# Kernel optimization log

Hardware: AMD Instinct MI355X
Metric: run time of the kernel (lower is better)

Reference implementation:

```python
import jax, jax.numpy as jnp
import numpy as np
from jax import lax

# model dims (must match init_kwargs)
NB, E, G0, G1 = 1, 64, 32, 256          # num_blocks, embed_dim, grid rows, grid cols
DM, DIN, DS, DC, DTR = 2048, 4096, 16, 4, 128  # d_model, d_inner, d_state, d_conv, dt_rank
PS, ST, KD = (2, 16), (2, 16), (31, 31)
B, C, T = 8, 64, 4096


def setup_inputs() -> dict:
    key = jax.random.key(0)
    ks = jax.random.split(key, 4)
    rng = np.random.default_rng(0)

    def w(*s, fan=None):
        fan = fan if fan is not None else s[-1]
        return jnp.asarray((rng.standard_normal(s) / np.sqrt(fan)).astype(np.float32))

    # mamba_ssm-style dt bias init: softplus(bias) ~ Uniform-log in [1e-3, 0.1]
    dt = np.exp(rng.uniform(size=(NB, 2, DIN)) * (np.log(0.1) - np.log(1e-3)) + np.log(1e-3))
    dt = np.clip(dt, 1e-4, None)
    bdt = jnp.asarray((dt + np.log(-np.expm1(-dt))).astype(np.float32))
    A_log = jnp.asarray(np.broadcast_to(np.log(np.arange(1, DS + 1, dtype=np.float32)), (NB, 2, DIN, DS)).copy())

    return {
        'x': jax.random.normal(ks[0], (B, C, T), dtype=jnp.float32),
        'mask': jax.random.uniform(ks[1], (B, C, T)) < 0.5,
        'proj_w': w(E, 1, PS[0], PS[1], fan=PS[0] * PS[1]),
        'proj_b': jnp.zeros((E,), jnp.float32),
        'pos_embed': 0.02 * jax.random.normal(ks[2], (1, G1, DM), dtype=jnp.float32),
        'in_proj_w': w(NB, 2, 2 * DIN, DM, fan=DM),
        'conv_w': w(NB, 2, DIN, DC, fan=DC),
        'conv_b': jnp.zeros((NB, 2, DIN), jnp.float32),
        'x_proj_w': w(NB, 2, DTR + 2 * DS, DIN, fan=DIN),
        'dt_proj_w': w(NB, 2, DIN, DTR, fan=DTR),
        'dt_proj_b': bdt,
        'A_log': A_log,
        'Dp': jnp.ones((NB, 2, DIN), jnp.float32),
        'out_proj_w': w(NB, 2, DM, DIN, fan=DIN),
        'ln_g': jnp.ones((NB, DM), jnp.float32),
        'ln_b': jnp.zeros((NB, DM), jnp.float32),
        'dec_conv_w': w(1, 1, KD[0], KD[1], fan=KD[0] * KD[1]),
        'convT_w': w(E, 1, PS[0], PS[1], fan=E),
        'convT_b': jnp.zeros((1,), jnp.float32),
    }


def _layernorm(x, g, b, eps=1e-5):
    m = jnp.mean(x, -1, keepdims=True)
    v = jnp.var(x, -1, keepdims=True)
    return (x - m) * lax.rsqrt(v + eps) * g + b


def _mamba(h, Win, Wc, bc, Wx, Wdt, bdt, Alog, Dp, Wout):
    # h: [B, L, DM]; faithful port of mamba_ssm Mamba (selective scan reference path)
    xz = jnp.einsum('bld,ed->ble', h, Win)               # [B, L, 2*DIN]
    xc, z = jnp.split(xz, 2, axis=-1)
    xc = xc.swapaxes(1, 2)                               # [B, DIN, L]
    xc = lax.conv_general_dilated(xc, Wc[:, None, :], (1,), ((DC - 1, 0),),
                                  dimension_numbers=('NCH', 'OIH', 'NCH'),
                                  feature_group_count=DIN) + bc[None, :, None]
    u = jax.nn.silu(xc).swapaxes(1, 2)                   # [B, L, DIN]
    x_dbl = jnp.einsum('bld,ed->ble', u, Wx)             # [B, L, DTR+2*DS]
    dt = jax.nn.softplus(jnp.einsum('blr,dr->bld', x_dbl[..., :DTR], Wdt) + bdt)
    Bm = x_dbl[..., DTR:DTR + DS]                        # [B, L, DS]
    Cm = x_dbl[..., DTR + DS:]                           # [B, L, DS]
    A = -jnp.exp(Alog)                                   # [DIN, DS]

    def step(hst, inp):
        dt_t, B_t, C_t, u_t = inp                        # [B,DIN],[B,DS],[B,DS],[B,DIN]
        dA = jnp.exp(dt_t[..., None] * A)                # [B, DIN, DS]
        hst = hst * dA + (dt_t * u_t)[..., None] * B_t[:, None, :]
        return hst, jnp.einsum('bds,bs->bd', hst, C_t)

    h0 = jnp.zeros((h.shape[0], DIN, DS), h.dtype)
    xs = (dt.swapaxes(0, 1), Bm.swapaxes(0, 1), Cm.swapaxes(0, 1), u.swapaxes(0, 1))
    _, ys = lax.scan(step, h0, xs)
    y = ys.swapaxes(0, 1) + u * Dp                       # [B, L, DIN]
    y = y * jax.nn.silu(z)
    return jnp.einsum('bld,ed->ble', y, Wout)            # [B, L, DM]


def _forward(x, mask, proj_w, proj_b, pos_embed, in_proj_w, conv_w, conv_b,
             x_proj_w, dt_proj_w, dt_proj_b, A_log, Dp, out_proj_w,
             ln_g, ln_b, dec_conv_w, convT_w, convT_b):
    xm = jnp.where(mask, 0.0, x)                         # x_masked[mask] = 0
    p = lax.conv_general_dilated(xm[:, None], proj_w, ST, 'VALID',
                                 dimension_numbers=('NCHW', 'OIHW', 'NCHW'))
    p = p + proj_b[None, :, None, None]                  # [B, E, G0, G1]
    h = p.reshape(p.shape[0], E * G0, G1).transpose(0, 2, 1) + pos_embed  # [B, G1, DM]
    for i in range(NB):
        a_f = (in_proj_w[i, 0], conv_w[i, 0], conv_b[i, 0], x_proj_w[i, 0], dt_proj_w[i, 0],
               dt_proj_b[i, 0], A_log[i, 0], Dp[i, 0], out_proj_w[i, 0])
        a_r = (in_proj_w[i, 1], conv_w[i, 1], conv_b[i, 1], x_proj_w[i, 1], dt_proj_w[i, 1],
               dt_proj_b[i, 1], A_log[i, 1], Dp[i, 1], out_proj_w[i, 1])
        o = _mamba(h, *a_f) + jnp.flip(_mamba(jnp.flip(h, 1), *a_r), 1)  # bidirectional add
        h = _layernorm(h + o, ln_g[i], ln_b[i])
    # Decoder
    d = lax.conv_general_dilated(h[:, None], dec_conv_w, (1, 1),
                                 (((KD[0] - 1) // 2,) * 2, ((KD[1] - 1) // 2,) * 2),
                                 dimension_numbers=('NCHW', 'OIHW', 'NCHW'))
    d = d[:, 0].transpose(0, 2, 1).reshape(-1, E, G0, G1)
    # ConvTranspose2d(E->1, k=PS, stride=ST) as lhs-dilated conv with flipped kernel
    wct = jnp.flip(convT_w, (2, 3)).swapaxes(0, 1)       # [1, E, kh, kw]
    rec = lax.conv_general_dilated(d, wct, (1, 1),
                                   ((PS[0] - 1, PS[0] - 1), (PS[1] - 1, PS[1] - 1)),
                                   lhs_dilation=ST,
                                   dimension_numbers=('NCHW', 'OIHW', 'NCHW'))
    rec = rec + convT_b[None, :, None, None]
    return rec[:, 0], x                                  # (x_reconstructed, x_original)


def reference(x, mask, proj_w, proj_b, pos_embed, in_proj_w, conv_w, conv_b,
              x_proj_w, dt_proj_w, dt_proj_b, A_log, Dp, out_proj_w,
              ln_g, ln_b, dec_conv_w, convT_w, convT_b):
    return _forward(x, mask, proj_w, proj_b, pos_embed, in_proj_w, conv_w, conv_b,
                    x_proj_w, dt_proj_w, dt_proj_b, A_log, Dp, out_proj_w,
                    ln_g, ln_b, dec_conv_w, convT_w, convT_b)
```

## Files before the change

kernel.cpp:

```cpp
#include <hip/hip_runtime.h>
#include <hip/hip_bf16.h>
#include <math.h>

typedef unsigned short u16;
typedef __attribute__((ext_vector_type(8))) short bf16x8;
typedef __attribute__((ext_vector_type(4))) float f32x4;

__device__ __forceinline__ float b2f(u16 v) {
  unsigned u = ((unsigned)v) << 16;
  return __builtin_bit_cast(float, u);
}
__device__ __forceinline__ u16 f2b(float f) {
  unsigned u = __builtin_bit_cast(unsigned, f);
  unsigned r = u + 0x7fffu + ((u >> 16) & 1u);
  return (u16)(r >> 16);
}
__device__ __forceinline__ void gload_lds16(const u16* g, u16* l) {
  __builtin_amdgcn_global_load_lds(
      (const __attribute__((address_space(1))) void*)g,
      (__attribute__((address_space(3))) void*)l, 16, 0, 0);
}

__global__ __launch_bounds__(256) void cvt_bf16_k(const float* __restrict__ s,
                                                  u16* __restrict__ d, int n4) {
  int i = blockIdx.x * 256 + threadIdx.x;
  if (i < n4) {
    float4 v = ((const float4*)s)[i];
    ushort4 o;
    o.x = f2b(v.x); o.y = f2b(v.y); o.z = f2b(v.z); o.w = f2b(v.w);
    ((ushort4*)d)[i] = o;
  }
}

__global__ __launch_bounds__(256) void toeplitz_k(
    const float* __restrict__ kw, u16* __restrict__ tb)
{
  int i = blockIdx.x * 256 + threadIdx.x;
  if (i >= 31744) return;
  int k = i & 31, n = (i >> 5) & 15, h = (i >> 9) & 1, ki = i >> 10;
  int t = h * 32 + k - n;
  float v = (t >= 0 && t <= 30) ? kw[ki * 31 + t] : 0.f;
  tb[i] = f2b(v);
}

__global__ __launch_bounds__(256) void patchify_k(
    const float* __restrict__ x, const int* __restrict__ mask,
    const float* __restrict__ pw, const float* __restrict__ pb,
    const float* __restrict__ pos, float* __restrict__ h, u16* __restrict__ hb)
{
  int g1 = blockIdx.x, b = blockIdx.y, tid = threadIdx.x;
  __shared__ float sX[64 * 17];
  __shared__ float sW[2048];
  for (int i = tid; i < 64 * 16; i += 256) {
    int r = i >> 4, c = i & 15;
    int gi = (b * 64 + r) * 4096 + g1 * 16 + c;
    sX[r * 17 + c] = mask[gi] ? 0.f : x[gi];
  }
  for (int i = tid; i < 2048; i += 256) sW[i] = pw[i];
  __syncthreads();
  for (int m = tid; m < 2048; m += 256) {
    int e = m >> 5, g0 = m & 31;
    float acc = pb[e];
    const float* w = &sW[e * 32];
#pragma unroll
    for (int kh = 0; kh < 2; ++kh)
#pragma unroll
      for (int kw = 0; kw < 16; ++kw)
        acc += sX[(2 * g0 + kh) * 17 + kw] * w[kh * 16 + kw];
    float v = acc + pos[g1 * 2048 + m];
    long o = ((long)b * 256 + g1) * 2048 + m;
    h[o] = v;
    hb[o] = f2b(v);
  }
}

__global__ __launch_bounds__(512, 2) void gemm256_k(
    const u16* __restrict__ A0,
    const u16* __restrict__ B0, long bStride,
    u16* __restrict__ C0, long cStride,
    const float* __restrict__ cw,
    const float* __restrict__ cb,
    u16* __restrict__ ub)
{
  constexpr int K = 2048, N = 8192, LDA = 2048;
  __shared__ __align__(16) u16 lds[67584];
  u16* As = lds;
  u16* Bs = lds + 32768;
  const int dir = blockIdx.z;
  const u16* A = A0;
  const u16* B = B0 + (long)dir * bStride;
  u16* C = C0 + (long)dir * cStride;
  const int flip = dir;

  const int tid = threadIdx.x;
  const int wave = tid >> 6, lane = tid & 63;
  const int wr = wave >> 2, wc = wave & 3;
  const int bm = blockIdx.y * 256, bn = blockIdx.x * 256;
  const int lr = lane & 15, lq = lane >> 4;

  f32x4 acc[8][4];
#pragma unroll
  for (int i = 0; i < 8; ++i)
#pragma unroll
    for (int j = 0; j < 4; ++j) acc[i][j] = (f32x4){0.f, 0.f, 0.f, 0.f};

  auto stage = [&](int buf, int kt) {
    int k0 = kt << 6;
#pragma unroll
    for (int hf = 0; hf < 2; ++hf)
#pragma unroll
      for (int j = 0; j < 2; ++j) {
        int g = j * 512 + tid;
        int rl = hf * 128 + (g >> 3);
        int gr = (g & 7) ^ ((g >> 3) & 7);
        int ar = flip ? (bm + 255 - rl) : (bm + rl);
        gload_lds16(A + (long)ar * LDA + k0 + gr * 8,
                    &As[buf * 16384 + hf * 8192 + g * 8]);
        gload_lds16(B + (long)(bn + rl) * K + k0 + gr * 8,
                    &Bs[buf * 16384 + hf * 8192 + g * 8]);
      }
  };

  const int nk = K >> 6;
  stage(0, 0);
  for (int kt = 0; kt < nk; ++kt) {
    __builtin_amdgcn_s_barrier();
    __builtin_amdgcn_sched_barrier(0);
    if (kt + 1 < nk) {
      stage((kt + 1) & 1, kt + 1);
      asm volatile("s_waitcnt vmcnt(16)" ::: "memory");
    } else {
      asm volatile("s_waitcnt vmcnt(0)" ::: "memory");
    }
    __builtin_amdgcn_sched_barrier(0);
    __builtin_amdgcn_s_barrier();
    __builtin_amdgcn_sched_barrier(0);
    const int buf = kt & 1;
#pragma unroll
    for (int h = 0; h < 2; ++h) {
      bf16x8 av[8], bv[4];
#pragma unroll
      for (int i = 0; i < 8; ++i) {
        int row = wr * 128 + i * 16 + lr;
        av[i] = *(const bf16x8*)
            &As[buf * 16384 + ((row * 64 + h * 32 + lq * 8) ^ ((row & 7) << 3))];
      }
#pragma unroll
      for (int j = 0; j < 4; ++j) {
        int row = wc * 64 + j * 16 + lr;
        bv[j] = *(const bf16x8*)
            &Bs[buf * 16384 + ((row * 64 + h * 32 + lq * 8) ^ ((row & 7) << 3))];
      }
      __builtin_amdgcn_s_setprio(1);
#pragma unroll
      for (int i = 0; i < 8; ++i)
#pragma unroll
        for (int j = 0; j < 4; ++j)
          acc[i][j] = __builtin_amdgcn_mfma_f32_16x16x32_bf16(
              av[i], bv[j], acc[i][j], 0, 0, 0);
      __builtin_amdgcn_s_setprio(0);
    }
  }

  if (bn < 4096) {
    __syncthreads();
    u16* tile = lds;
#pragma unroll
    for (int i = 0; i < 8; ++i) {
      int r0 = wr * 128 + i * 16 + lq * 4;
#pragma unroll
      for (int j = 0; j < 4; ++j) {
        int col = wc * 64 + j * 16 + lr;
        f32x4 v = acc[i][j];
#pragma unroll
        for (int r = 0; r < 4; ++r)
          tile[(r0 + r) * 264 + col] = f2b(v[r]);
      }
    }
    __syncthreads();
    const int rgrp = tid >> 5, c8 = tid & 31;
    const int d0 = bn + c8 * 8;
    float wv0[8], wv1[8], wv2[8], wv3[8], cbv[8];
#pragma unroll
    for (int e = 0; e < 8; ++e) {
      const float4 wq = *(const float4*)(cw + ((long)dir * 4096 + d0 + e) * 4);
      wv0[e] = wq.x; wv1[e] = wq.y; wv2[e] = wq.z; wv3[e] = wq.w;
      cbv[e] = cb[dir * 4096 + d0 + e];
    }
    const int l0 = rgrp * 16;
    float w0[8], w1[8], w2[8];
#pragma unroll
    for (int e = 0; e < 8; ++e) { w0[e] = 0.f; w1[e] = 0.f; w2[e] = 0.f; }
    if (rgrp > 0) {
      bf16x8 t0 = *(const bf16x8*)&tile[(l0 - 3) * 264 + c8 * 8];
      bf16x8 t1 = *(const bf16x8*)&tile[(l0 - 2) * 264 + c8 * 8];
      bf16x8 t2 = *(const bf16x8*)&tile[(l0 - 1) * 264 + c8 * 8];
#pragma unroll
      for (int e = 0; e < 8; ++e) {
        w0[e] = b2f((u16)t0[e]); w1[e] = b2f((u16)t1[e]); w2[e] = b2f((u16)t2[e]);
      }
    }
    long ubase = ((long)(dir * 8 + blockIdx.y) * 256 + l0) * 4096 + d0;
#pragma unroll
    for (int l = 0; l < 16; ++l) {
      bf16x8 t = *(const bf16x8*)&tile[(l0 + l) * 264 + c8 * 8];
      float cur[8];
#pragma unroll
      for (int e = 0; e < 8; ++e) cur[e] = b2f((u16)t[e]);
      bf16x8 ov;
#pragma unroll
      for (int e = 0; e < 8; ++e) {
        float a = cbv[e] + wv0[e] * w0[e] + wv1[e] * w1[e] + wv2[e] * w2[e] +
                  wv3[e] * cur[e];
        ov[e] = (short)f2b(a / (1.f + __expf(-a)));
      }
      *(bf16x8*)(ub + ubase + (long)l * 4096) = ov;
#pragma unroll
      for (int e = 0; e < 8; ++e) { w0[e] = w1[e]; w1[e] = w2[e]; w2[e] = cur[e]; }
    }
  } else {
#pragma unroll
    for (int i = 0; i < 8; ++i) {
      int r0 = bm + wr * 128 + i * 16 + lq * 4;
#pragma unroll
      for (int j = 0; j < 4; ++j) {
        int col = bn + wc * 64 + j * 16 + lr;
        f32x4 v = acc[i][j];
#pragma unroll
        for (int r = 0; r < 4; ++r)
          C[(long)(r0 + r) * N + col] = f2b(v[r]);
      }
    }
  }
}

__global__ __launch_bounds__(512, 2) void gemm256o_k(
    const u16* __restrict__ Y0,
    const u16* __restrict__ W0,
    float* __restrict__ part)
{
  constexpr int LDK = 4096;
  __shared__ __align__(16) u16 lds[65536];
  u16* As = lds;
  u16* Bs = lds + 32768;
  const int dir = blockIdx.z >> 1, split = blockIdx.z & 1;
  const u16* A = Y0 + (long)dir * 2048 * 4096;
  const u16* B = W0 + (long)dir * 2048 * 4096;
  float* C = part + (long)blockIdx.z * 4194304;
  const int kbase = split << 11;

  const int tid = threadIdx.x;
  const int wave = tid >> 6, lane = tid & 63;
  const int wr = wave >> 2, wc = wave & 3;
  const int bm = blockIdx.y * 256, bn = blockIdx.x * 256;
  const int lr = lane & 15, lq = lane >> 4;

  f32x4 acc[8][4];
#pragma unroll
  for (int i = 0; i < 8; ++i)
#pragma unroll
    for (int j = 0; j < 4; ++j) acc[i][j] = (f32x4){0.f, 0.f, 0.f, 0.f};

  auto stage = [&](int buf, int kt) {
    int k0 = kbase + (kt << 6);
#pragma unroll
    for (int hf = 0; hf < 2; ++hf)
#pragma unroll
      for (int j = 0; j < 2; ++j) {
        int g = j * 512 + tid;
        int rl = hf * 128 + (g >> 3);
        int gr = (g & 7) ^ ((g >> 3) & 7);
        gload_lds16(A + (long)(bm + rl) * LDK + k0 + gr * 8,
                    &As[buf * 16384 + hf * 8192 + g * 8]);
        gload_lds16(B + (long)(bn + rl) * LDK + k0 + gr * 8,
                    &Bs[buf * 16384 + hf * 8192 + g * 8]);
      }
  };

  const int nk = 32;
  stage(0, 0);
  for (int kt = 0; kt < nk; ++kt) {
    __builtin_amdgcn_s_barrier();
    __builtin_amdgcn_sched_barrier(0);
    if (kt + 1 < nk) {
      stage((kt + 1) & 1, kt + 1);
      asm volatile("s_waitcnt vmcnt(16)" ::: "memory");
    } else {
      asm volatile("s_waitcnt vmcnt(0)" ::: "memory");
    }
    __builtin_amdgcn_sched_barrier(0);
    __builtin_amdgcn_s_barrier();
    __builtin_amdgcn_sched_barrier(0);
    const int buf = kt & 1;
#pragma unroll
    for (int h = 0; h < 2; ++h) {
      bf16x8 av[8], bv[4];
#pragma unroll
      for (int i = 0; i < 8; ++i) {
        int row = wr * 128 + i * 16 + lr;
        av[i] = *(const bf16x8*)
            &As[buf * 16384 + ((row * 64 + h * 32 + lq * 8) ^ ((row & 7) << 3))];
      }
#pragma unroll
      for (int j = 0; j < 4; ++j) {
        int row = wc * 64 + j * 16 + lr;
        bv[j] = *(const bf16x8*)
            &Bs[buf * 16384 + ((row * 64 + h * 32 + lq * 8) ^ ((row & 7) << 3))];
      }
      __builtin_amdgcn_s_setprio(1);
#pragma unroll
      for (int i = 0; i < 8; ++i)
#pragma unroll
        for (int j = 0; j < 4; ++j)
          acc[i][j] = __builtin_amdgcn_mfma_f32_16x16x32_bf16(
              av[i], bv[j], acc[i][j], 0, 0, 0);
      __builtin_amdgcn_s_setprio(0);
    }
  }

#pragma unroll
  for (int i = 0; i < 8; ++i) {
    int r0 = bm + wr * 128 + i * 16 + lq * 4;
#pragma unroll
    for (int j = 0; j < 4; ++j) {
      int col = bn + wc * 64 + j * 16 + lr;
      f32x4 v = acc[i][j];
#pragma unroll
      for (int r = 0; r < 4; ++r)
        C[(long)(r0 + r) * 2048 + col] = v[r];
    }
  }
}

__global__ __launch_bounds__(256) void oproj_reduce_k(
    const float* __restrict__ part, float* __restrict__ ob)
{
  int i = blockIdx.x * 256 + threadIdx.x;
  if (i >= 2097152) return;
  int dir = i >> 20, rem = i & 1048575;
  const float4* p0 = (const float4*)(part + (long)(dir * 2) * 4194304) + rem;
  const float4* p1 = (const float4*)(part + (long)(dir * 2 + 1) * 4194304) + rem;
  float4 a = *p0, b = *p1;
  ((float4*)(ob + (long)dir * 4194304))[rem] =
      make_float4(a.x + b.x, a.y + b.y, a.z + b.z, a.w + b.w);
}

template <int EPI, int F32OUT, int BFOUT>
__global__ __launch_bounds__(256) void mfma_gemm_k(
    const u16* __restrict__ A0, long aStride,
    const u16* __restrict__ B0, long bStride,
    float* __restrict__ C0, long cStride,
    u16* __restrict__ Cb0, long cbStride,
    const float* __restrict__ bias0, int biasStride,
    int N, int K, int lda, int flipDir1)
{
  __shared__ __align__(16) u16 As[2][4096];
  __shared__ __align__(16) u16 Bs[2][4096];
  const int dir = blockIdx.z;
  const u16* A = A0 + (long)dir * aStride;
  const u16* B = B0 + (long)dir * bStride;
  float* C = F32OUT ? (C0 + (long)dir * cStride) : nullptr;
  u16* Cb = BFOUT ? (Cb0 + (long)dir * cbStride) : nullptr;
  const float* bias = (EPI == 1) ? (bias0 + (long)dir * biasStride) : nullptr;
  const int flip = flipDir1 && (dir == 1);

  const int tid = threadIdx.x;
  const int wave = tid >> 6, lane = tid & 63;
  const int wr = wave >> 1, wc = wave & 1;
  const int bm = blockIdx.y * 128, bn = blockIdx.x * 128;
  const int lr = lane & 15, lq = lane >> 4;

  f32x4 acc[4][4];
#pragma unroll
  for (int i = 0; i < 4; ++i)
#pragma unroll
    for (int j = 0; j < 4; ++j) acc[i][j] = (f32x4){0.f, 0.f, 0.f, 0.f};

  const int nk = K >> 5;

  auto stage = [&](int buf, int k0) {
#pragma unroll
    for (int iss = 0; iss < 2; ++iss) {
      int ob = wave * 2048 + iss * 1024 + lane * 16;
      int row = ob >> 6, kb = (ob >> 4) & 3;
      int rg = bm + row;
      rg = flip ? ((rg & ~255) | (255 - (rg & 255))) : rg;
      gload_lds16(A + (long)rg * lda + k0 + kb * 8,
                  &As[buf][wave * 1024 + iss * 512]);
      int rb = bn + row; rb = (rb < N) ? rb : (N - 1);
      gload_lds16(B + (long)rb * K + k0 + kb * 8,
                  &Bs[buf][wave * 1024 + iss * 512]);
    }
  };

  stage(0, 0);
  for (int kt = 0; kt < nk; ++kt) {
    __syncthreads();
    if (kt + 1 < nk) stage((kt + 1) & 1, (kt + 1) << 5);
    const int buf = kt & 1;
    bf16x8 av[4], bv[4];
#pragma unroll
    for (int i = 0; i < 4; ++i)
      av[i] = *(const bf16x8*)&As[buf][(wr * 64 + i * 16 + lr) * 32 + lq * 8];
#pragma unroll
    for (int j = 0; j < 4; ++j)
      bv[j] = *(const bf16x8*)&Bs[buf][(wc * 64 + j * 16 + lr) * 32 + lq * 8];
#pragma unroll
    for (int i = 0; i < 4; ++i)
#pragma unroll
      for (int j = 0; j < 4; ++j)
        acc[i][j] = __builtin_amdgcn_mfma_f32_16x16x32_bf16(av[i], bv[j],
                                                            acc[i][j], 0, 0, 0);
  }

#pragma unroll
  for (int i = 0; i < 4; ++i) {
    int r0 = bm + wr * 64 + i * 16 + lq * 4;
#pragma unroll
    for (int j = 0; j < 4; ++j) {
      int col = bn + wc * 64 + j * 16 + lr;
      if (col < N) {
        f32x4 v = acc[i][j];
#pragma unroll
        for (int r = 0; r < 4; ++r) {
          float xv = v[r];
          if (EPI == 1) {
            xv += bias[col];
            xv = (xv > 20.f) ? xv : log1pf(expf(xv));
          }
          if (F32OUT) C[(long)(r0 + r) * N + col] = xv;
          if (BFOUT) Cb[(long)(r0 + r) * N + col] = f2b(xv);
        }
      }
    }
  }
}

__global__ __launch_bounds__(256) void xdbl_part_k(
    const u16* __restrict__ ubf, const u16* __restrict__ Wxbf,
    float* __restrict__ part)
{
  __shared__ __align__(16) u16 As[2][4096];
  __shared__ __align__(16) u16 Bs[2][4096];
  const int dir = blockIdx.z >> 2, split = blockIdx.z & 3;
  const u16* A = ubf + (long)dir * 2048 * 4096;
  const u16* B = Wxbf + (long)dir * 160 * 4096;
  float* C = part + (long)blockIdx.z * 327680;
  const int tid = threadIdx.x;
  const int wave = tid >> 6, lane = tid & 63;
  const int wr = wave >> 1, wc = wave & 1;
  const int bm = blockIdx.y * 128, bn = blockIdx.x * 128;
  const int lr = lane & 15, lq = lane >> 4;

  f32x4 acc[4][4];
#pragma unroll
  for (int i = 0; i < 4; ++i)
#pragma unroll
    for (int j = 0; j < 4; ++j) acc[i][j] = (f32x4){0.f, 0.f, 0.f, 0.f};

  auto stage = [&](int buf, int k0) {
#pragma unroll
    for (int iss = 0; iss < 2; ++iss) {
      int ob = wave * 2048 + iss * 1024 + lane * 16;
      int row = ob >> 6, kb = (ob >> 4) & 3;
      gload_lds16(A + (long)(bm + row) * 4096 + k0 + kb * 8,
                  &As[buf][wave * 1024 + iss * 512]);
      int rb = bn + row; rb = (rb < 160) ? rb : 159;
      gload_lds16(B + (long)rb * 4096 + k0 + kb * 8,
                  &Bs[buf][wave * 1024 + iss * 512]);
    }
  };

  const int kbase = split << 10;
  stage(0, kbase);
  for (int kt = 0; kt < 32; ++kt) {
    __syncthreads();
    if (kt + 1 < 32) stage((kt + 1) & 1, kbase + ((kt + 1) << 5));
    const int buf = kt & 1;
    bf16x8 av[4], bv[4];
#pragma unroll
    for (int i = 0; i < 4; ++i)
      av[i] = *(const bf16x8*)&As[buf][(wr * 64 + i * 16 + lr) * 32 + lq * 8];
#pragma unroll
    for (int j = 0; j < 4; ++j)
      bv[j] = *(const bf16x8*)&Bs[buf][(wc * 64 + j * 16 + lr) * 32 + lq * 8];
#pragma unroll
    for (int i = 0; i < 4; ++i)
#pragma unroll
      for (int j = 0; j < 4; ++j)
        acc[i][j] = __builtin_amdgcn_mfma_f32_16x16x32_bf16(av[i], bv[j],
                                                            acc[i][j], 0, 0, 0);
  }

#pragma unroll
  for (int i = 0; i < 4; ++i) {
    int r0 = bm + wr * 64 + i * 16 + lq * 4;
#pragma unroll
    for (int j = 0; j < 4; ++j) {
      int col = bn + wc * 64 + j * 16 + lr;
      if (col < 160) {
        f32x4 v = acc[i][j];
#pragma unroll
        for (int r = 0; r < 4; ++r)
          C[(long)(r0 + r) * 160 + col] = v[r];
      }
    }
  }
}

__global__ __launch_bounds__(256) void xdbl_reduce_k(
    const float* __restrict__ part, float* __restrict__ xdbl,
    u16* __restrict__ xdbl_bf)
{
  int i = blockIdx.x * 256 + threadIdx.x;
  if (i >= 655360) return;
  int dir = i / 327680, rem = i - dir * 327680;
  long pb = (long)dir * 4 * 327680 + rem;
  float s = part[pb] + part[pb + 327680] + part[pb + 2 * 327680] +
            part[pb + 3 * 327680];
  xdbl[i] = s;
  xdbl_bf[i] = f2b(s);
}

__global__ __launch_bounds__(256) void scan_a_k(
    const u16* __restrict__ dtbuf, const u16* __restrict__ ubuf,
    const float* __restrict__ xdbl, const float* __restrict__ A_log,
    const float* __restrict__ Dpv, u16* __restrict__ ypre,
    float* __restrict__ stend, float* __restrict__ dtsum)
{
  int blk = blockIdx.x;
  int dtile = blk & 15, c = (blk >> 4) & 7, b = (blk >> 7) & 7, dir = blk >> 10;
  int tid = threadIdx.x;
  int d = dtile * 256 + tid;
  int db = dir * 8 + b;

  __shared__ float sB[32][16], sC[32][16];
  long r160 = (long)db * 256 * 160;
  for (int i = tid; i < 1024; i += 256) {
    int l = i >> 5, s = i & 31;
    float v = xdbl[r160 + (long)(c * 32 + l) * 160 + 128 + s];
    if (s < 16) sB[l][s] = v; else sC[l][s - 16] = v;
  }
  __syncthreads();

  float A[16], st[16];
  const float4* ap = (const float4*)(A_log + ((long)dir * 4096 + d) * 16);
#pragma unroll
  for (int q = 0; q < 4; ++q) {
    float4 t = ap[q];
    A[q * 4 + 0] = -__expf(t.x); A[q * 4 + 1] = -__expf(t.y);
    A[q * 4 + 2] = -__expf(t.z); A[q * 4 + 3] = -__expf(t.w);
  }
#pragma unroll
  for (int s = 0; s < 16; ++s) st[s] = 0.f;
  float Dpd = Dpv[dir * 4096 + d];

  long base = (long)db * 256 * 4096 + (long)c * 32 * 4096 + d;
  float dts = 0.f;
  for (int i = 0; i < 32; ++i) {
    float dtv = b2f(dtbuf[base + (long)i * 4096]);
    float uv  = b2f(ubuf[base + (long)i * 4096]);
    dts += dtv;
    float du = dtv * uv;
    float y = 0.f;
#pragma unroll
    for (int s = 0; s < 16; ++s) {
      st[s] = st[s] * __expf(dtv * A[s]) + du * sB[i][s];
      y += st[s] * sC[i][s];
    }
    ypre[base + (long)i * 4096] = f2b(y + uv * Dpd);
  }
  long eb = ((long)(db * 8 + c) * 4096 + d) * 16;
  float4* ep = (float4*)(stend + eb);
#pragma unroll
  for (int q = 0; q < 4; ++q)
    ep[q] = make_float4(st[q * 4], st[q * 4 + 1], st[q * 4 + 2], st[q * 4 + 3]);
  dtsum[(long)(db * 8 + c) * 4096 + d] = dts;
}

__global__ __launch_bounds__(512) void scan_b_k(
    const u16* __restrict__ dtbuf, const u16* __restrict__ xzbf,
    const float* __restrict__ xdbl, const float* __restrict__ A_log,
    const float* __restrict__ stend, const float* __restrict__ dtsum,
    u16* __restrict__ ybuf)
{
  int blk = blockIdx.x;
  int dtile = blk & 63, b = (blk >> 6) & 7, dir = blk >> 9;
  int tid = threadIdx.x;
  int c = tid >> 6, dd = tid & 63;
  int d0 = dtile * 64, d = d0 + dd;
  int db = dir * 8 + b;

  __shared__ float sEnd[8][64][17];
  __shared__ float sT[8][64];
  __shared__ float sC[256][16];

  long eBase = (long)db * 8 * 65536;
  for (int i = tid; i < 8192; i += 512) {
    int cc = i >> 10, rem = i & 1023, dd2 = rem >> 4, s = rem & 15;
    sEnd[cc][dd2][s] = stend[eBase + (long)cc * 65536 + (long)(d0 + dd2) * 16 + s];
  }
  {
    int cc = tid >> 6, dd2 = tid & 63;
    sT[cc][dd2] = dtsum[(long)(db * 8 + cc) * 4096 + d0 + dd2];
  }
  long r160 = (long)db * 256 * 160;
  for (int i = tid; i < 4096; i += 512) {
    int l = i >> 4, s = i & 15;
    sC[l][s] = xdbl[r160 + (long)l * 160 + 144 + s];
  }
  __syncthreads();

  float A[16];
  const float4* ap = (const float4*)(A_log + ((long)dir * 4096 + d) * 16);
#pragma unroll
  for (int q = 0; q < 4; ++q) {
    float4 t = ap[q];
    A[q * 4 + 0] = -__expf(t.x); A[q * 4 + 1] = -__expf(t.y);
    A[q * 4 + 2] = -__expf(t.z); A[q * 4 + 3] = -__expf(t.w);
  }
  float g[16];
#pragma unroll
  for (int s = 0; s < 16; ++s) g[s] = 0.f;
  for (int j = 0; j < c; ++j) {
    float Tj = sT[j][dd];
#pragma unroll
    for (int s = 0; s < 16; ++s)
      g[s] = g[s] * __expf(A[s] * Tj) + sEnd[j][dd][s];
  }

  long base  = (long)db * 256 * 4096 + (long)c * 32 * 4096 + d;
  long zbase = (long)db * 256 * 8192 + (long)c * 32 * 8192 + 4096 + d;
  float cum = 0.f;
  if (c == 0) {
    for (int i = 0; i < 32; ++i) {
      float yp = b2f(ybuf[base + (long)i * 4096]);
      float zv = b2f(xzbf[zbase + (long)i * 8192]);
      float y = yp * (zv / (1.f + __expf(-zv)));
      ybuf[base + (long)i * 4096] = f2b(y);
    }
  } else {
    for (int i = 0; i < 32; ++i) {
      float dtv = b2f(dtbuf[base + (long)i * 4096]);
      cum += dtv;
      float yp = b2f(ybuf[base + (long)i * 4096]);
      float corr = 0.f;
      const int l = c * 32 + i;
#pragma unroll
      for (int s = 0; s < 16; ++s)
        corr += sC[l][s] * __expf(A[s] * cum) * g[s];
      float zv = b2f(xzbf[zbase + (long)i * 8192]);
      float y = (yp + corr) * (zv / (1.f + __expf(-zv)));
      ybuf[base + (long)i * 4096] = f2b(y);
    }
  }
}

__global__ __launch_bounds__(256) void add_ln_k(
    const float* __restrict__ h, const float* __restrict__ o0,
    const float* __restrict__ o1, const float* __restrict__ g,
    const float* __restrict__ bta, float* __restrict__ h2)
{
  int row = blockIdx.x;
  int b = row >> 8, l = row & 255;
  long base = (long)row * 2048;
  long base1 = ((long)b * 256 + (255 - l)) * 2048;
  int t8 = threadIdx.x * 8;
  float v[8];
  float4 x0 = *(const float4*)(h + base + t8);
  float4 x1 = *(const float4*)(h + base + t8 + 4);
  float4 a0 = *(const float4*)(o0 + base + t8);
  float4 a1 = *(const float4*)(o0 + base + t8 + 4);
  float4 c0 = *(const float4*)(o1 + base1 + t8);
  float4 c1 = *(const float4*)(o1 + base1 + t8 + 4);
  v[0] = x0.x + a0.x + c0.x; v[1] = x0.y + a0.y + c0.y;
  v[2] = x0.z + a0.z + c0.z; v[3] = x0.w + a0.w + c0.w;
  v[4] = x1.x + a1.x + c1.x; v[5] = x1.y + a1.y + c1.y;
  v[6] = x1.z + a1.z + c1.z; v[7] = x1.w + a1.w + c1.w;
  float s = 0.f, ss = 0.f;
#pragma unroll
  for (int j = 0; j < 8; ++j) { s += v[j]; ss += v[j] * v[j]; }
#pragma unroll
  for (int off = 32; off >= 1; off >>= 1) {
    s += __shfl_xor(s, off, 64);
    ss += __shfl_xor(ss, off, 64);
  }
  __shared__ float red[8];
  int wid = threadIdx.x >> 6, lane = threadIdx.x & 63;
  if (lane == 0) { red[wid] = s; red[wid + 4] = ss; }
  __syncthreads();
  if (threadIdx.x == 0) {
    red[0] = red[0] + red[1] + red[2] + red[3];
    red[4] = red[4] + red[5] + red[6] + red[7];
  }
  __syncthreads();
  float mean = red[0] * (1.f / 2048.f);
  float var = red[4] * (1.f / 2048.f) - mean * mean;
  float inv = rsqrtf(var + 1e-5f);
  float o[8];
#pragma unroll
  for (int j = 0; j < 8; ++j)
    o[j] = (v[j] - mean) * inv * g[t8 + j] + bta[t8 + j];
  *(float4*)(h2 + base + t8) = make_float4(o[0], o[1], o[2], o[3]);
  *(float4*)(h2 + base + t8 + 4) = make_float4(o[4], o[5], o[6], o[7]);
}

__global__ __launch_bounds__(256) void dec_conv31_k(
    const float* __restrict__ h2, const u16* __restrict__ tb,
    float* __restrict__ dc)
{
  __shared__ __align__(16) u16 sIn[94 * 120];
  const int b = blockIdx.z;
  const int l0 = blockIdx.y * 64;
  const int m0 = blockIdx.x * 64;
  const int tid = threadIdx.x;
  const float* src = h2 + (long)b * 256 * 2048;
  for (int i = tid; i < 94 * 112; i += 256) {
    int r = i / 112, c = i - r * 112;
    int gl = l0 + r - 15, gm = m0 + c - 15;
    float v = 0.f;
    if (gl >= 0 && gl < 256 && gm >= 0 && gm < 2048)
      v = src[(long)gl * 2048 + gm];
    sIn[r * 120 + c] = f2b(v);
  }
  __syncthreads();
  const int wave = tid >> 6, lane = tid & 63;
  const int lr = lane & 15, lq = lane >> 4;

  f32x4 acc[4];
#pragma unroll
  for (int s = 0; s < 4; ++s) acc[s] = (f32x4){0.f, 0.f, 0.f, 0.f};

#pragma unroll 1
  for (int ki = 0; ki < 31; ++ki) {
    const u16* arow = &sIn[(wave * 16 + lr + ki) * 120];
#pragma unroll
    for (int h = 0; h < 2; ++h) {
      bf16x8 bv = *(const bf16x8*)&tb[((ki * 2 + h) * 16 + lr) * 32 + lq * 8];
#pragma unroll
      for (int ms = 0; ms < 4; ++ms) {
        bf16x8 av = *(const bf16x8*)&arow[ms * 16 + h * 32 + lq * 8];
        acc[ms] = __builtin_amdgcn_mfma_f32_16x16x32_bf16(av, bv, acc[ms], 0, 0, 0);
      }
    }
  }
#pragma unroll
  for (int ms = 0; ms < 4; ++ms) {
    f32x4 v = acc[ms];
#pragma unroll
    for (int r = 0; r < 4; ++r)
      dc[((long)b * 256 + l0 + wave * 16 + lq * 4 + r) * 2048 + m0 + ms * 16 + lr]
          = v[r];
  }
}

__global__ __launch_bounds__(256) void convT_k(
    const float* __restrict__ dc, const float* __restrict__ w,
    const float* __restrict__ wb, float* __restrict__ out)
{
  int j = blockIdx.x, b = blockIdx.y;
  __shared__ float sD[2048];
  __shared__ float sW[2048];
  int tid = threadIdx.x;
  const float* drow = dc + ((long)b * 256 + j) * 2048;
  for (int i = tid; i < 2048; i += 256) { sD[i] = drow[i]; sW[i] = w[i]; }
  __syncthreads();
  float cb = wb[0];
  int owlo = tid & 15, ohbase = tid >> 4;
#pragma unroll
  for (int q = 0; q < 4; ++q) {
    int oh = ohbase + q * 16;
    int i = oh >> 1, a = oh & 1;
    float acc = cb;
#pragma unroll 8
    for (int e = 0; e < 64; ++e)
      acc += sD[e * 32 + i] * sW[e * 32 + a * 16 + owlo];
    out[((long)b * 64 + oh) * 4096 + j * 16 + owlo] = acc;
  }
}

extern "C" void kernel_launch(void* const* d_in, const int* in_sizes, int n_in,
                              void* d_out, int out_size, void* d_ws, size_t ws_size,
                              hipStream_t stream)
{
  const float* x      = (const float*)d_in[0];
  const int*   mask   = (const int*)d_in[1];
  const float* proj_w = (const float*)d_in[2];
  const float* proj_b = (const float*)d_in[3];
  const float* pos    = (const float*)d_in[4];
  const float* Wip    = (const float*)d_in[5];
  const float* convw  = (const float*)d_in[6];
  const float* convb  = (const float*)d_in[7];
  const float* Wx     = (const float*)d_in[8];
  const float* Wdt    = (const float*)d_in[9];
  const float* bdt    = (const float*)d_in[10];
  const float* Alog   = (const float*)d_in[11];
  const float* Dpv    = (const float*)d_in[12];
  const float* Wout   = (const float*)d_in[13];
  const float* lng    = (const float*)d_in[14];
  const float* lnb    = (const float*)d_in[15];
  const float* dkw    = (const float*)d_in[16];
  const float* ctw    = (const float*)d_in[17];
  const float* ctb    = (const float*)d_in[18];
  float* out = (float*)d_out;

  char* p = (char*)d_ws;
  u16*   xz_bf   = (u16*)p;
  float* ob      = (float*)p;
  p += 67108864;
  u16*   u_bf    = (u16*)p;
  float* dc      = (float*)p;
  p += 33554432;
  u16*   dt_bf   = (u16*)p; p += 67108864;
  float* xdbl    = (float*)p; p += 2621440;
  u16*   xdbl_bf = (u16*)p;  p += 1310720;
  float* h       = (float*)p; p += 16777216;
  u16*   h_bf    = (u16*)p;  p += 8388608;
  float* h2      = (float*)p; p += 16777216;
  u16*   y_bf    = (u16*)p;  p += 33554432;
  u16*   Wpool   = (u16*)p;  p += 67108864;
  u16*   Wx_bf   = (u16*)p;  p += 2621440;
  u16*   Wdt_bf  = (u16*)p;  p += 2097152;
  u16*   tb      = (u16*)p;  p += 65536;

  float* part    = (float*)(Wpool + 16777216);
  float* st_end  = (float*)(Wpool + 16777216);
  float* dtsum   = h2;
  float* opart   = (float*)dt_bf;

  cvt_bf16_k<<<32768, 256, 0, stream>>>(Wip, Wpool, 8388608);
  cvt_bf16_k<<<1280, 256, 0, stream>>>(Wx, Wx_bf, 327680);
  cvt_bf16_k<<<1024, 256, 0, stream>>>(Wdt, Wdt_bf, 262144);
  toeplitz_k<<<124, 256, 0, stream>>>(dkw, tb);

  patchify_k<<<dim3(256, 8), 256, 0, stream>>>(x, mask, proj_w, proj_b, pos, h, h_bf);

  gemm256_k<<<dim3(32, 8, 2), 512, 0, stream>>>(
      h_bf, Wpool, (long)8192 * 2048, xz_bf, (long)2048 * 8192,
      convw, convb, u_bf);

  xdbl_part_k<<<dim3(2, 16, 8), 256, 0, stream>>>(u_bf, Wx_bf, part);
  xdbl_reduce_k<<<2560, 256, 0, stream>>>(part, xdbl, xdbl_bf);

  mfma_gemm_k<1, 0, 1><<<dim3(32, 16, 2), 256, 0, stream>>>(
      xdbl_bf, (long)2048 * 160, Wdt_bf, (long)4096 * 128, nullptr, 0L,
      dt_bf, (long)2048 * 4096, bdt, 4096, 4096, 128, 160, 0);

  scan_a_k<<<2048, 256, 0, stream>>>(dt_bf, u_bf, xdbl, Alog, Dpv, y_bf, st_end, dtsum);
  scan_b_k<<<1024, 512, 0, stream>>>(dt_bf, xz_bf, xdbl, Alog, st_end, dtsum, y_bf);

  cvt_bf16_k<<<16384, 256, 0, stream>>>(Wout, Wpool, 4194304);

  gemm256o_k<<<dim3(8, 8, 4), 512, 0, stream>>>(y_bf, Wpool, opart);
  oproj_reduce_k<<<8192, 256, 0, stream>>>(opart, ob);

  add_ln_k<<<2048, 256, 0, stream>>>(h, ob, ob + (long)2048 * 2048, lng, lnb, h2);

  dec_conv31_k<<<dim3(32, 4, 8), 256, 0, stream>>>(h2, tb, dc);

  convT_k<<<dim3(256, 8), 256, 0, stream>>>(dc, ctw, ctb, out);

  hipMemcpyAsync(out + 2097152, x, (size_t)2097152 * 4,
                 hipMemcpyDeviceToDevice, stream);
}
```

Before: 623.9 us.

## Halve in-proj GEMM LDS tile, fuse o-proj split-K reduce into layernorm, bf16 LN output

The in-proj GEMM now stages K-tiles of 32 instead of 64 with a new swizzle, which halves its shared memory so more blocks can be resident per CU. Its conv/SiLU epilogue is split into two halves, with a small side buffer carrying the three boundary rows between them. The separate o-proj partial-sum reduce kernel is removed, and the layernorm now reads all four partial buffers directly. The layernorm also writes bf16, which the decoder conv loads without converting. The trade-off is twice as many K-loop iterations and barriers in the GEMM, plus an extra synchronization phase in the epilogue.

```diff
diff --git a/kernel.cpp b/kernel.cpp
--- a/kernel.cpp
+++ b/kernel.cpp
@@ -83,9 +83,9 @@
     u16* __restrict__ ub)
 {
   constexpr int K = 2048, N = 8192, LDA = 2048;
-  __shared__ __align__(16) u16 lds[67584];
+  __shared__ __align__(16) u16 lds[34584];
   u16* As = lds;
-  u16* Bs = lds + 32768;
+  u16* Bs = lds + 16384;
   const int dir = blockIdx.z;
   const u16* A = A0;
   const u16* B = B0 + (long)dir * bStride;
@@ -105,30 +105,27 @@
     for (int j = 0; j < 4; ++j) acc[i][j] = (f32x4){0.f, 0.f, 0.f, 0.f};
 
   auto stage = [&](int buf, int kt) {
-    int k0 = kt << 6;
-#pragma unroll
-    for (int hf = 0; hf < 2; ++hf)
-#pragma unroll
-      for (int j = 0; j < 2; ++j) {
-        int g = j * 512 + tid;
-        int rl = hf * 128 + (g >> 3);
-        int gr = (g & 7) ^ ((g >> 3) & 7);
-        int ar = flip ? (bm + 255 - rl) : (bm + rl);
-        gload_lds16(A + (long)ar * LDA + k0 + gr * 8,
-                    &As[buf * 16384 + hf * 8192 + g * 8]);
-        gload_lds16(B + (long)(bn + rl) * K + k0 + gr * 8,
-                    &Bs[buf * 16384 + hf * 8192 + g * 8]);
-      }
+    int k0 = kt << 5;
+#pragma unroll
+    for (int j = 0; j < 2; ++j) {
+      int g = j * 512 + tid;
+      int row = g >> 2, sp = g & 3;
+      int ss = sp ^ (row & 3) ^ (((row >> 2) & 1) << 1);
+      int ar = flip ? (bm + 255 - row) : (bm + row);
+      gload_lds16(A + (long)ar * LDA + k0 + ss * 8, &As[buf * 8192 + g * 8]);
+      gload_lds16(B + (long)(bn + row) * K + k0 + ss * 8,
+                  &Bs[buf * 8192 + g * 8]);
+    }
   };
 
-  const int nk = K >> 6;
+  const int nk = K >> 5;
   stage(0, 0);
   for (int kt = 0; kt < nk; ++kt) {
     __builtin_amdgcn_s_barrier();
     __builtin_amdgcn_sched_barrier(0);
     if (kt + 1 < nk) {
       stage((kt + 1) & 1, kt + 1);
-      asm volatile("s_waitcnt vmcnt(16)" ::: "memory");
+      asm volatile("s_waitcnt vmcnt(4)" ::: "memory");
     } else {
       asm volatile("s_waitcnt vmcnt(0)" ::: "memory");
     }
@@ -136,48 +133,32 @@
     __builtin_amdgcn_s_barrier();
     __builtin_amdgcn_sched_barrier(0);
     const int buf = kt & 1;
-#pragma unroll
-    for (int h = 0; h < 2; ++h) {
-      bf16x8 av[8], bv[4];
-#pragma unroll
-      for (int i = 0; i < 8; ++i) {
-        int row = wr * 128 + i * 16 + lr;
-        av[i] = *(const bf16x8*)
-            &As[buf * 16384 + ((row * 64 + h * 32 + lq * 8) ^ ((row & 7) << 3))];
-      }
-#pragma unroll
-      for (int j = 0; j < 4; ++j) {
-        int row = wc * 64 + j * 16 + lr;
-        bv[j] = *(const bf16x8*)
-            &Bs[buf * 16384 + ((row * 64 + h * 32 + lq * 8) ^ ((row & 7) << 3))];
-      }
-      __builtin_amdgcn_s_setprio(1);
-#pragma unroll
-      for (int i = 0; i < 8; ++i)
-#pragma unroll
-        for (int j = 0; j < 4; ++j)
-          acc[i][j] = __builtin_amdgcn_mfma_f32_16x16x32_bf16(
-              av[i], bv[j], acc[i][j], 0, 0, 0);
-      __builtin_amdgcn_s_setprio(0);
-    }
+    bf16x8 av[8], bv[4];
+#pragma unroll
+    for (int i = 0; i < 8; ++i) {
+      int R = wr * 128 + i * 16 + lr;
+      int gp = lq ^ (R & 3) ^ (((R >> 2) & 1) << 1);
+      av[i] = *(const bf16x8*)&As[buf * 8192 + R * 32 + gp * 8];
+    }
+#pragma unroll
+    for (int j = 0; j < 4; ++j) {
+      int R = wc * 64 + j * 16 + lr;
+      int gp = lq ^ (R & 3) ^ (((R >> 2) & 1) << 1);
+      bv[j] = *(const bf16x8*)&Bs[buf * 8192 + R * 32 + gp * 8];
+    }
+    __builtin_amdgcn_s_setprio(1);
+#pragma unroll
+    for (int i = 0; i < 8; ++i)
+#pragma unroll
+      for (int j = 0; j < 4; ++j)
+        acc[i][j] = __builtin_amdgcn_mfma_f32_16x16x32_bf16(
+            av[i], bv[j], acc[i][j], 0, 0, 0);
+    __builtin_amdgcn_s_setprio(0);
   }
 
   if (bn < 4096) {
-    __syncthreads();
     u16* tile = lds;
-#pragma unroll
-    for (int i = 0; i < 8; ++i) {
-      int r0 = wr * 128 + i * 16 + lq * 4;
-#pragma unroll
-      for (int j = 0; j < 4; ++j) {
-        int col = wc * 64 + j * 16 + lr;
-        f32x4 v = acc[i][j];
-#pragma unroll
-        for (int r = 0; r < 4; ++r)
-          tile[(r0 + r) * 264 + col] = f2b(v[r]);
-      }
-    }
-    __syncthreads();
+    u16* side = lds + 33792;
     const int rgrp = tid >> 5, c8 = tid & 31;
     const int d0 = bn + c8 * 8;
     float wv0[8], wv1[8], wv2[8], wv3[8], cbv[8];
@@ -187,37 +168,83 @@
       wv0[e] = wq.x; wv1[e] = wq.y; wv2[e] = wq.z; wv3[e] = wq.w;
       cbv[e] = cb[dir * 4096 + d0 + e];
     }
-    const int l0 = rgrp * 16;
     float w0[8], w1[8], w2[8];
-#pragma unroll
-    for (int e = 0; e < 8; ++e) { w0[e] = 0.f; w1[e] = 0.f; w2[e] = 0.f; }
-    if (rgrp > 0) {
-      bf16x8 t0 = *(const bf16x8*)&tile[(l0 - 3) * 264 + c8 * 8];
-      bf16x8 t1 = *(const bf16x8*)&tile[(l0 - 2) * 264 + c8 * 8];
-      bf16x8 t2 = *(const bf16x8*)&tile[(l0 - 1) * 264 + c8 * 8];
-#pragma unroll
-      for (int e = 0; e < 8; ++e) {
-        w0[e] = b2f((u16)t0[e]); w1[e] = b2f((u16)t1[e]); w2[e] = b2f((u16)t2[e]);
-      }
-    }
-    long ubase = ((long)(dir * 8 + blockIdx.y) * 256 + l0) * 4096 + d0;
-#pragma unroll
-    for (int l = 0; l < 16; ++l) {
-      bf16x8 t = *(const bf16x8*)&tile[(l0 + l) * 264 + c8 * 8];
-      float cur[8];
-#pragma unroll
-      for (int e = 0; e < 8; ++e) cur[e] = b2f((u16)t[e]);
-      bf16x8 ov;
-#pragma unroll
-      for (int e = 0; e < 8; ++e) {
-        float a = cbv[e] + wv0[e] * w0[e] + wv1[e] * w1[e] + wv2[e] * w2[e] +
-                  wv3[e] * cur[e];
-        ov[e] = (short)f2b(a / (1.f + __expf(-a)));
-      }
-      *(bf16x8*)(ub + ubase + (long)l * 4096) = ov;
-#pragma unroll
-      for (int e = 0; e < 8; ++e) { w0[e] = w1[e]; w1[e] = w2[e]; w2[e] = cur[e]; }
-    }
+
+    auto writeacc = [&]() {
+#pragma unroll
+      for (int i = 0; i < 8; ++i) {
+        int r0 = i * 16 + lq * 4;
+#pragma unroll
+        for (int j = 0; j < 4; ++j) {
+          int col = wc * 64 + j * 16 + lr;
+          f32x4 v = acc[i][j];
+#pragma unroll
+          for (int r = 0; r < 4; ++r)
+            tile[(r0 + r) * 264 + col] = f2b(v[r]);
+        }
+      }
+    };
+
+    auto convhalf = [&](int hh) {
+      if (rgrp == 0) {
+        if (hh == 0) {
+#pragma unroll
+          for (int e = 0; e < 8; ++e) { w0[e] = 0.f; w1[e] = 0.f; w2[e] = 0.f; }
+        } else {
+          bf16x8 t0 = *(const bf16x8*)&side[0 * 264 + c8 * 8];
+          bf16x8 t1 = *(const bf16x8*)&side[1 * 264 + c8 * 8];
+          bf16x8 t2 = *(const bf16x8*)&side[2 * 264 + c8 * 8];
+#pragma unroll
+          for (int e = 0; e < 8; ++e) {
+            w0[e] = b2f((u16)t0[e]); w1[e] = b2f((u16)t1[e]);
+            w2[e] = b2f((u16)t2[e]);
+          }
+        }
+      } else {
+        int lb = rgrp * 8;
+        bf16x8 t0 = *(const bf16x8*)&tile[(lb - 3) * 264 + c8 * 8];
+        bf16x8 t1 = *(const bf16x8*)&tile[(lb - 2) * 264 + c8 * 8];
+        bf16x8 t2 = *(const bf16x8*)&tile[(lb - 1) * 264 + c8 * 8];
+#pragma unroll
+        for (int e = 0; e < 8; ++e) {
+          w0[e] = b2f((u16)t0[e]); w1[e] = b2f((u16)t1[e]);
+          w2[e] = b2f((u16)t2[e]);
+        }
+      }
+      long ubase = ((long)(dir * 8 + blockIdx.y) * 256 + hh * 128 + rgrp * 8)
+                       * 4096 + d0;
+#pragma unroll
+      for (int l = 0; l < 8; ++l) {
+        bf16x8 t = *(const bf16x8*)&tile[(rgrp * 8 + l) * 264 + c8 * 8];
+        float cur[8];
+#pragma unroll
+        for (int e = 0; e < 8; ++e) cur[e] = b2f((u16)t[e]);
+        bf16x8 ov;
+#pragma unroll
+        for (int e = 0; e < 8; ++e) {
+          float a = cbv[e] + wv0[e] * w0[e] + wv1[e] * w1[e] + wv2[e] * w2[e] +
+                    wv3[e] * cur[e];
+          ov[e] = (short)f2b(a / (1.f + __expf(-a)));
+        }
+        *(bf16x8*)(ub + ubase + (long)l * 4096) = ov;
+#pragma unroll
+        for (int e = 0; e < 8; ++e) { w0[e] = w1[e]; w1[e] = w2[e]; w2[e] = cur[e]; }
+      }
+    };
+
+    __syncthreads();
+    if (wr == 0) writeacc();
+    __syncthreads();
+    convhalf(0);
+    if (tid < 96) {
+      int rr = tid >> 5, cc = tid & 31;
+      *(bf16x8*)&side[rr * 264 + cc * 8] =
+          *(const bf16x8*)&tile[(125 + rr) * 264 + cc * 8];
+    }
+    __syncthreads();
+    if (wr == 1) writeacc();
+    __syncthreads();
+    convhalf(1);
   } else {
 #pragma unroll
     for (int i = 0; i < 8; ++i) {
@@ -330,19 +357,6 @@
         C[(long)(r0 + r) * 2048 + col] = v[r];
     }
   }
-}
-
-__global__ __launch_bounds__(256) void oproj_reduce_k(
-    const float* __restrict__ part, float* __restrict__ ob)
-{
-  int i = blockIdx.x * 256 + threadIdx.x;
-  if (i >= 2097152) return;
-  int dir = i >> 20, rem = i & 1048575;
-  const float4* p0 = (const float4*)(part + (long)(dir * 2) * 4194304) + rem;
-  const float4* p1 = (const float4*)(part + (long)(dir * 2 + 1) * 4194304) + rem;
-  float4 a = *p0, b = *p1;
-  ((float4*)(ob + (long)dir * 4194304))[rem] =
-      make_float4(a.x + b.x, a.y + b.y, a.z + b.z, a.w + b.w);
 }
 
 template <int EPI, int F32OUT, int BFOUT>
@@ -657,26 +671,38 @@
 }
 
 __global__ __launch_bounds__(256) void add_ln_k(
-    const float* __restrict__ h, const float* __restrict__ o0,
-    const float* __restrict__ o1, const float* __restrict__ g,
-    const float* __restrict__ bta, float* __restrict__ h2)
+    const float* __restrict__ h, const float* __restrict__ op,
+    const float* __restrict__ g, const float* __restrict__ bta,
+    u16* __restrict__ h2b)
 {
   int row = blockIdx.x;
   int b = row >> 8, l = row & 255;
   long base = (long)row * 2048;
   long base1 = ((long)b * 256 + (255 - l)) * 2048;
   int t8 = threadIdx.x * 8;
+  const float* p0 = op;
+  const float* p1 = op + 4194304;
+  const float* p2 = op + 2L * 4194304;
+  const float* p3 = op + 3L * 4194304;
   float v[8];
   float4 x0 = *(const float4*)(h + base + t8);
   float4 x1 = *(const float4*)(h + base + t8 + 4);
-  float4 a0 = *(const float4*)(o0 + base + t8);
-  float4 a1 = *(const float4*)(o0 + base + t8 + 4);
-  float4 c0 = *(const float4*)(o1 + base1 + t8);
-  float4 c1 = *(const float4*)(o1 + base1 + t8 + 4);
-  v[0] = x0.x + a0.x + c0.x; v[1] = x0.y + a0.y + c0.y;
-  v[2] = x0.z + a0.z + c0.z; v[3] = x0.w + a0.w + c0.w;
-  v[4] = x1.x + a1.x + c1.x; v[5] = x1.y + a1.y + c1.y;
-  v[6] = x1.z + a1.z + c1.z; v[7] = x1.w + a1.w + c1.w;
+  float4 a0 = *(const float4*)(p0 + base + t8);
+  float4 a1 = *(const float4*)(p0 + base + t8 + 4);
+  float4 b0 = *(const float4*)(p1 + base + t8);
+  float4 b1 = *(const float4*)(p1 + base + t8 + 4);
+  float4 c0 = *(const float4*)(p2 + base1 + t8);
+  float4 c1 = *(const float4*)(p2 + base1 + t8 + 4);
+  float4 d0 = *(const float4*)(p3 + base1 + t8);
+  float4 d1 = *(const float4*)(p3 + base1 + t8 + 4);
+  v[0] = x0.x + a0.x + b0.x + c0.x + d0.x;
+  v[1] = x0.y + a0.y + b0.y + c0.y + d0.y;
+  v[2] = x0.z + a0.z + b0.z + c0.z + d0.z;
+  v[3] = x0.w + a0.w + b0.w + c0.w + d0.w;
+  v[4] = x1.x + a1.x + b1.x + c1.x + d1.x;
+  v[5] = x1.y + a1.y + b1.y + c1.y + d1.y;
+  v[6] = x1.z + a1.z + b1.z + c1.z + d1.z;
+  v[7] = x1.w + a1.w + b1.w + c1.w + d1.w;
   float s = 0.f, ss = 0.f;
 #pragma unroll
   for (int j = 0; j < 8; ++j) { s += v[j]; ss += v[j] * v[j]; }
@@ -697,16 +723,15 @@
   float mean = red[0] * (1.f / 2048.f);
   float var = red[4] * (1.f / 2048.f) - mean * mean;
   float inv = rsqrtf(var + 1e-5f);
-  float o[8];
+  bf16x8 o;
 #pragma unroll
   for (int j = 0; j < 8; ++j)
-    o[j] = (v[j] - mean) * inv * g[t8 + j] + bta[t8 + j];
-  *(float4*)(h2 + base + t8) = make_float4(o[0], o[1], o[2], o[3]);
-  *(float4*)(h2 + base + t8 + 4) = make_float4(o[4], o[5], o[6], o[7]);
+    o[j] = (short)f2b((v[j] - mean) * inv * g[t8 + j] + bta[t8 + j]);
+  *(bf16x8*)(h2b + base + t8) = o;
 }
 
 __global__ __launch_bounds__(256) void dec_conv31_k(
-    const float* __restrict__ h2, const u16* __restrict__ tb,
+    const u16* __restrict__ h2b, const u16* __restrict__ tb,
     float* __restrict__ dc)
 {
   __shared__ __align__(16) u16 sIn[94 * 120];
@@ -714,14 +739,14 @@
   const int l0 = blockIdx.y * 64;
   const int m0 = blockIdx.x * 64;
   const int tid = threadIdx.x;
-  const float* src = h2 + (long)b * 256 * 2048;
+  const u16* src = h2b + (long)b * 256 * 2048;
   for (int i = tid; i < 94 * 112; i += 256) {
     int r = i / 112, c = i - r * 112;
     int gl = l0 + r - 15, gm = m0 + c - 15;
-    float v = 0.f;
+    u16 v = 0;
     if (gl >= 0 && gl < 256 && gm >= 0 && gm < 2048)
       v = src[(long)gl * 2048 + gm];
-    sIn[r * 120 + c] = f2b(v);
+    sIn[r * 120 + c] = v;
   }
   __syncthreads();
   const int wave = tid >> 6, lane = tid & 63;
@@ -806,7 +831,6 @@
 
   char* p = (char*)d_ws;
   u16*   xz_bf   = (u16*)p;
-  float* ob      = (float*)p;
   p += 67108864;
   u16*   u_bf    = (u16*)p;
   float* dc      = (float*)p;
@@ -822,6 +846,7 @@
   u16*   Wx_bf   = (u16*)p;  p += 2621440;
   u16*   Wdt_bf  = (u16*)p;  p += 2097152;
   u16*   tb      = (u16*)p;  p += 65536;
+  u16*   h2b     = (u16*)p;  p += 8388608;
 
   float* part    = (float*)(Wpool + 16777216);
   float* st_end  = (float*)(Wpool + 16777216);
@@ -852,11 +877,10 @@
   cvt_bf16_k<<<16384, 256, 0, stream>>>(Wout, Wpool, 4194304);
 
   gemm256o_k<<<dim3(8, 8, 4), 512, 0, stream>>>(y_bf, Wpool, opart);
-  oproj_reduce_k<<<8192, 256, 0, stream>>>(opart, ob);
-
-  add_ln_k<<<2048, 256, 0, stream>>>(h, ob, ob + (long)2048 * 2048, lng, lnb, h2);
-
-  dec_conv31_k<<<dim3(32, 4, 8), 256, 0, stream>>>(h2, tb, dc);
+
+  add_ln_k<<<2048, 256, 0, stream>>>(h, opart, lng, lnb, h2b);
+
+  dec_conv31_k<<<dim3(32, 4, 8), 256, 0, stream>>>(h2b, tb, dc);
 
   convT_k<<<dim3(256, 8), 256, 0, stream>>>(dc, ctw, ctb, out);
 
```

Result: no change. 616.6 us (-1.2%).

## Write out-proj partials as bf16 and fold split-K reduce into add+LayerNorm

Applied to the files above, without the earlier changes.

The split-K out-projection GEMM now stores its four partial outputs in bf16 instead of fp32. The separate reduce kernel is removed, and add_ln_k sums the residual plus all four partials directly. LayerNorm output is written as bf16, so the decoder conv loads bf16 without converting. This cuts one launch and several tens of MB of fp32 memory traffic, at the cost of extra rounding on the partial sums and on the LayerNorm output.

```diff
diff --git a/kernel.cpp b/kernel.cpp
--- a/kernel.cpp
+++ b/kernel.cpp
@@ -237,7 +237,7 @@
 __global__ __launch_bounds__(512, 2) void gemm256o_k(
     const u16* __restrict__ Y0,
     const u16* __restrict__ W0,
-    float* __restrict__ part)
+    u16* __restrict__ part)
 {
   constexpr int LDK = 4096;
   __shared__ __align__(16) u16 lds[65536];
@@ -246,7 +246,7 @@
   const int dir = blockIdx.z >> 1, split = blockIdx.z & 1;
   const u16* A = Y0 + (long)dir * 2048 * 4096;
   const u16* B = W0 + (long)dir * 2048 * 4096;
-  float* C = part + (long)blockIdx.z * 4194304;
+  u16* C = part + (long)blockIdx.z * 4194304;
   const int kbase = split << 11;
 
   const int tid = threadIdx.x;
@@ -327,22 +327,9 @@
       f32x4 v = acc[i][j];
 #pragma unroll
       for (int r = 0; r < 4; ++r)
-        C[(long)(r0 + r) * 2048 + col] = v[r];
-    }
-  }
-}
-
-__global__ __launch_bounds__(256) void oproj_reduce_k(
-    const float* __restrict__ part, float* __restrict__ ob)
-{
-  int i = blockIdx.x * 256 + threadIdx.x;
-  if (i >= 2097152) return;
-  int dir = i >> 20, rem = i & 1048575;
-  const float4* p0 = (const float4*)(part + (long)(dir * 2) * 4194304) + rem;
-  const float4* p1 = (const float4*)(part + (long)(dir * 2 + 1) * 4194304) + rem;
-  float4 a = *p0, b = *p1;
-  ((float4*)(ob + (long)dir * 4194304))[rem] =
-      make_float4(a.x + b.x, a.y + b.y, a.z + b.z, a.w + b.w);
+        C[(long)(r0 + r) * 2048 + col] = f2b(v[r]);
+    }
+  }
 }
 
 template <int EPI, int F32OUT, int BFOUT>
@@ -657,26 +644,33 @@
 }
 
 __global__ __launch_bounds__(256) void add_ln_k(
-    const float* __restrict__ h, const float* __restrict__ o0,
-    const float* __restrict__ o1, const float* __restrict__ g,
-    const float* __restrict__ bta, float* __restrict__ h2)
+    const float* __restrict__ h, const u16* __restrict__ op,
+    const float* __restrict__ g, const float* __restrict__ bta,
+    u16* __restrict__ h2b)
 {
   int row = blockIdx.x;
   int b = row >> 8, l = row & 255;
   long base = (long)row * 2048;
   long base1 = ((long)b * 256 + (255 - l)) * 2048;
   int t8 = threadIdx.x * 8;
+  const u16* p0 = op;
+  const u16* p1 = op + 4194304;
+  const u16* p2 = op + 2L * 4194304;
+  const u16* p3 = op + 3L * 4194304;
   float v[8];
   float4 x0 = *(const float4*)(h + base + t8);
   float4 x1 = *(const float4*)(h + base + t8 + 4);
-  float4 a0 = *(const float4*)(o0 + base + t8);
-  float4 a1 = *(const float4*)(o0 + base + t8 + 4);
-  float4 c0 = *(const float4*)(o1 + base1 + t8);
-  float4 c1 = *(const float4*)(o1 + base1 + t8 + 4);
-  v[0] = x0.x + a0.x + c0.x; v[1] = x0.y + a0.y + c0.y;
-  v[2] = x0.z + a0.z + c0.z; v[3] = x0.w + a0.w + c0.w;
-  v[4] = x1.x + a1.x + c1.x; v[5] = x1.y + a1.y + c1.y;
-  v[6] = x1.z + a1.z + c1.z; v[7] = x1.w + a1.w + c1.w;
+  bf16x8 a8 = *(const bf16x8*)(p0 + base + t8);
+  bf16x8 b8 = *(const bf16x8*)(p1 + base + t8);
+  bf16x8 c8v = *(const bf16x8*)(p2 + base1 + t8);
+  bf16x8 d8 = *(const bf16x8*)(p3 + base1 + t8);
+  const float* xp = (const float*)&x0;
+  float xv[8] = {x0.x, x0.y, x0.z, x0.w, x1.x, x1.y, x1.z, x1.w};
+  (void)xp;
+#pragma unroll
+  for (int j = 0; j < 8; ++j)
+    v[j] = xv[j] + b2f((u16)a8[j]) + b2f((u16)b8[j]) + b2f((u16)c8v[j]) +
+           b2f((u16)d8[j]);
   float s = 0.f, ss = 0.f;
 #pragma unroll
   for (int j = 0; j < 8; ++j) { s += v[j]; ss += v[j] * v[j]; }
@@ -697,16 +691,15 @@
   float mean = red[0] * (1.f / 2048.f);
   float var = red[4] * (1.f / 2048.f) - mean * mean;
   float inv = rsqrtf(var + 1e-5f);
-  float o[8];
+  bf16x8 o;
 #pragma unroll
   for (int j = 0; j < 8; ++j)
-    o[j] = (v[j] - mean) * inv * g[t8 + j] + bta[t8 + j];
-  *(float4*)(h2 + base + t8) = make_float4(o[0], o[1], o[2], o[3]);
-  *(float4*)(h2 + base + t8 + 4) = make_float4(o[4], o[5], o[6], o[7]);
+    o[j] = (short)f2b((v[j] - mean) * inv * g[t8 + j] + bta[t8 + j]);
+  *(bf16x8*)(h2b + base + t8) = o;
 }
 
 __global__ __launch_bounds__(256) void dec_conv31_k(
-    const float* __restrict__ h2, const u16* __restrict__ tb,
+    const u16* __restrict__ h2b, const u16* __restrict__ tb,
     float* __restrict__ dc)
 {
   __shared__ __align__(16) u16 sIn[94 * 120];
@@ -714,14 +707,14 @@
   const int l0 = blockIdx.y * 64;
   const int m0 = blockIdx.x * 64;
   const int tid = threadIdx.x;
-  const float* src = h2 + (long)b * 256 * 2048;
+  const u16* src = h2b + (long)b * 256 * 2048;
   for (int i = tid; i < 94 * 112; i += 256) {
     int r = i / 112, c = i - r * 112;
     int gl = l0 + r - 15, gm = m0 + c - 15;
-    float v = 0.f;
+    u16 v = 0;
     if (gl >= 0 && gl < 256 && gm >= 0 && gm < 2048)
       v = src[(long)gl * 2048 + gm];
-    sIn[r * 120 + c] = f2b(v);
+    sIn[r * 120 + c] = v;
   }
   __syncthreads();
   const int wave = tid >> 6, lane = tid & 63;
@@ -806,7 +799,6 @@
 
   char* p = (char*)d_ws;
   u16*   xz_bf   = (u16*)p;
-  float* ob      = (float*)p;
   p += 67108864;
   u16*   u_bf    = (u16*)p;
   float* dc      = (float*)p;
@@ -822,11 +814,12 @@
   u16*   Wx_bf   = (u16*)p;  p += 2621440;
   u16*   Wdt_bf  = (u16*)p;  p += 2097152;
   u16*   tb      = (u16*)p;  p += 65536;
+  u16*   h2b     = (u16*)p;  p += 8388608;
 
   float* part    = (float*)(Wpool + 16777216);
   float* st_end  = (float*)(Wpool + 16777216);
   float* dtsum   = h2;
-  float* opart   = (float*)dt_bf;
+  u16*   opart   = dt_bf;
 
   cvt_bf16_k<<<32768, 256, 0, stream>>>(Wip, Wpool, 8388608);
   cvt_bf16_k<<<1280, 256, 0, stream>>>(Wx, Wx_bf, 327680);
@@ -852,11 +845,10 @@
   cvt_bf16_k<<<16384, 256, 0, stream>>>(Wout, Wpool, 4194304);
 
   gemm256o_k<<<dim3(8, 8, 4), 512, 0, stream>>>(y_bf, Wpool, opart);
-  oproj_reduce_k<<<8192, 256, 0, stream>>>(opart, ob);
-
-  add_ln_k<<<2048, 256, 0, stream>>>(h, ob, ob + (long)2048 * 2048, lng, lnb, h2);
-
-  dec_conv31_k<<<dim3(32, 4, 8), 256, 0, stream>>>(h2, tb, dc);
+
+  add_ln_k<<<2048, 256, 0, stream>>>(h, opart, lng, lnb, h2b);
+
+  dec_conv31_k<<<dim3(32, 4, 8), 256, 0, stream>>>(h2b, tb, dc);
 
   convT_k<<<dim3(256, 8), 256, 0, stream>>>(dc, ctw, ctb, out);
 
```

Measured after the change: 593.5 us. 4.9% less time.
